# Optimization experiments

Measured on AMD Instinct MI355X. Metric: run time of the kernel, lower is better.

## Reference

```python
import jax, jax.numpy as jnp
import numpy as np

N = 100000
IN_DIM = 128
OUT_DIM = 128
E = 3200000


def setup_inputs() -> dict:
    key = jax.random.key(0)
    k1, k2, k3, k4, k5 = jax.random.split(key, 5)
    x = jax.random.normal(k1, (N, IN_DIM), dtype=jnp.float32)
    src = jax.random.randint(k2, (E,), 0, N)
    dst = jax.random.randint(k3, (E,), 0, N)
    edge_index = jnp.stack([src, dst], axis=0)  # (2, E) int
    # Linear(2*in_dim, out_dim): torch stores weight as (out, in)
    bound = 1.0 / np.sqrt(2 * IN_DIM)
    W = jax.random.uniform(k4, (OUT_DIM, 2 * IN_DIM), minval=-bound, maxval=bound, dtype=jnp.float32)
    b = jax.random.uniform(k5, (OUT_DIM,), minval=-bound, maxval=bound, dtype=jnp.float32)
    return {"x": x, "edge_index": edge_index, "W": W, "b": b}


def reference(x, edge_index, W, b):
    # x: (N, d), edge_index: (2, E)
    n = x.shape[0]
    src, dst = edge_index[0], edge_index[1]
    # scatter-add of source features into target buckets (mean aggregation)
    agg = jax.ops.segment_sum(x[src], dst, num_segments=n)          # (N, d)
    count = jax.ops.segment_sum(jnp.ones((src.shape[0],), x.dtype), dst, num_segments=n)
    count = jnp.maximum(count, 1.0)[:, None]                         # (N, 1)
    neigh_mean = agg / count
    combined = jnp.concatenate([x, neigh_mean], axis=1)              # (N, 2d)
    return combined @ W.T + b
```

## Files before the change

kernel.cpp:

```cpp
#include <hip/hip_runtime.h>

typedef unsigned int u32;
typedef unsigned short u16;
typedef unsigned char u8;
typedef _Float16 half8 __attribute__((ext_vector_type(8)));
typedef float f32x4 __attribute__((ext_vector_type(4)));
typedef float f32x2 __attribute__((ext_vector_type(2)));

#define STRIDE 16384

__global__ __launch_bounds__(256) void part_k(const int* __restrict__ src, const int* __restrict__ dst,
                                              int E, u32* __restrict__ cnt,
                                              u32* __restrict__ packed, int nbkt,
                                              const float* __restrict__ x, u16* __restrict__ xh,
                                              u32* __restrict__ xq,
                                              const float* __restrict__ W, u16* __restrict__ wh,
                                              int N, int nba, int nbx) {
  int b = blockIdx.x, tid = threadIdx.x;
  if (b < nba) {
    __shared__ u32 h[512];
    for (int t = tid; t < 512; t += 256) h[t] = 0u;
    __syncthreads();
    int base = b * 8192;
    for (int it = 0; it < 32; it++) {
      int i = base + it * 256 + tid;
      if (i < E) atomicAdd(&h[(u32)dst[i] >> 8], 1u);
    }
    __syncthreads();
    for (int t = tid; t < nbkt; t += 256) {
      u32 c = h[t];
      h[t] = c ? atomicAdd(&cnt[t], c) : 0u;
    }
    __syncthreads();
    for (int it = 0; it < 32; it++) {
      int i = base + it * 256 + tid;
      if (i < E) {
        u32 d = (u32)dst[i];
        u32 pos = atomicAdd(&h[d >> 8], 1u);
        if (pos < (u32)STRIDE)
          packed[(size_t)(d >> 8) * STRIDE + pos] = (u32)src[i] | ((d & 255u) << 24);
      }
    }
  } else if (b < nba + nbx) {
    int i = (b - nba) * 256 + tid;
    if (i < N * 32) {
      const float4 v = *(const float4*)(x + (size_t)i * 4);
      u32 p0 = __builtin_bit_cast(u32, __builtin_amdgcn_cvt_pkrtz(v.x, v.y));
      u32 p1 = __builtin_bit_cast(u32, __builtin_amdgcn_cvt_pkrtz(v.z, v.w));
      *(uint2*)(xh + (size_t)i * 4) = uint2{p0, p1};
      u32 q = 0;
      q = __builtin_amdgcn_cvt_pk_fp8_f32(v.x, v.y, q, false);
      q = __builtin_amdgcn_cvt_pk_fp8_f32(v.z, v.w, q, true);
      xq[i] = q;
    }
  } else {
    int i = (b - nba - nbx) * 256 + tid;
    if (i < 8192) {
      const float4 v = *(const float4*)(W + (size_t)i * 4);
      u32 p0 = __builtin_bit_cast(u32, __builtin_amdgcn_cvt_pkrtz(v.x, v.y));
      u32 p1 = __builtin_bit_cast(u32, __builtin_amdgcn_cvt_pkrtz(v.z, v.w));
      *(uint2*)(wh + (size_t)i * 4) = uint2{p0, p1};
    }
  }
}

__global__ __launch_bounds__(256) void bucket_k(const u32* __restrict__ packed,
                                                const u32* __restrict__ cnt, int N,
                                                u32* __restrict__ offsets, int* __restrict__ ssrc,
                                                u8* __restrict__ nodeperm) {
  __shared__ u32 c256[256];
  __shared__ u32 scn[256];
  __shared__ u32 cur[256];
  int b = blockIdx.x, t = threadIdx.x;
  size_t fb = (size_t)b * STRIDE;
  u32 cb = cnt[b]; if (cb > (u32)STRIDE) cb = (u32)STRIDE;
  c256[t] = 0u;
  __syncthreads();
  for (u32 j = t; j < cb; j += 256) atomicAdd(&c256[packed[fb + j] >> 24], 1u);
  __syncthreads();
  u32 v = c256[t];
  scn[t] = v;
  __syncthreads();
  for (int off = 1; off < 256; off <<= 1) {
    u32 x = (t >= off) ? scn[t - off] : 0u;
    __syncthreads();
    scn[t] += x;
    __syncthreads();
  }
  u32 lbase = scn[t] - v;
  int node = b * 256 + t;
  int lastT = N - 1 - b * 256; if (lastT > 255) lastT = 255;
  u32* orow = offsets + (size_t)b * 257;
  if (node < N) {
    orow[t] = (u32)(fb + lbase);
    if (t == lastT) orow[t + 1] = (u32)(fb + lbase + v);
  }
  cur[t] = lbase;
  __syncthreads();
  for (u32 j = t; j < cb; j += 256) {
    u32 w = packed[fb + j];
    u32 pos = atomicAdd(&cur[w >> 24], 1u);
    ssrc[fb + pos] = (int)(w & 0xFFFFFFu);
  }
  {
    int g = t >> 5, l = t & 31;
    u32 mykey = c256[t] * 256u + (u32)l;
    const u32* cg = &c256[g * 32];
    u32 rank = 0;
#pragma unroll 8
    for (int l2 = 0; l2 < 32; l2++) {
      u32 k2 = cg[l2] * 256u + (u32)l2;
      rank += (k2 < mykey) ? 1u : 0u;
    }
    nodeperm[(size_t)b * 256 + g * 32 + rank] = (u8)l;
  }
}

#define DECV(vv, A0, A1, A2, A3) { f32x2 p;                              \
    p = __builtin_amdgcn_cvt_pk_f32_fp8((vv).x, false); A0 += p;         \
    p = __builtin_amdgcn_cvt_pk_f32_fp8((vv).x, true);  A1 += p;         \
    p = __builtin_amdgcn_cvt_pk_f32_fp8((vv).y, false); A2 += p;         \
    p = __builtin_amdgcn_cvt_pk_f32_fp8((vv).y, true);  A3 += p; }

__global__ __launch_bounds__(256) void fuse_k(const int* __restrict__ ssrc,
                                              const u32* __restrict__ offsets,
                                              const u32* __restrict__ xq,
                                              const u16* __restrict__ xh,
                                              const u16* __restrict__ wh,
                                              const float* __restrict__ bias,
                                              const u8* __restrict__ nodeperm,
                                              float* __restrict__ out, int N) {
  __shared__ u16 mlds[32][136];
  int wv = threadIdx.x >> 6, lane = threadIdx.x & 63;
  int sub = lane >> 4, cl = lane & 15;
  int nbase = blockIdx.x * 32;

  for (int r = 0; r < 2; r++) {
    int ln = nodeperm[(size_t)nbase + r * 16 + wv * 4 + sub];
    int node = nbase + ln;
    f32x2 A0{0.f,0.f}, A1{0.f,0.f}, A2{0.f,0.f}, A3{0.f,0.f};
    u32 deg = 0;
    if (node < N) {
      size_t oi = (size_t)(node >> 8) * 257 + (node & 255);
      u32 s0 = offsets[oi], s1 = offsets[oi + 1];
      deg = s1 - s0;
      u32 j = s0;
      u32 nq = deg >> 2;
      if (nq) {
        uint4 iA = *(const uint4*)(ssrc + j);
        for (u32 q = 1; q < nq; q++) {
          uint4 iN = *(const uint4*)(ssrc + j + 4);
          uint2 v0 = *(const uint2*)(xq + ((size_t)iA.x << 5) + (cl << 1));
          uint2 v1 = *(const uint2*)(xq + ((size_t)iA.y << 5) + (cl << 1));
          uint2 v2 = *(const uint2*)(xq + ((size_t)iA.z << 5) + (cl << 1));
          uint2 v3 = *(const uint2*)(xq + ((size_t)iA.w << 5) + (cl << 1));
          DECV(v0, A0, A1, A2, A3) DECV(v1, A0, A1, A2, A3)
          DECV(v2, A0, A1, A2, A3) DECV(v3, A0, A1, A2, A3)
          iA = iN; j += 4;
        }
        {
          uint2 v0 = *(const uint2*)(xq + ((size_t)iA.x << 5) + (cl << 1));
          uint2 v1 = *(const uint2*)(xq + ((size_t)iA.y << 5) + (cl << 1));
          uint2 v2 = *(const uint2*)(xq + ((size_t)iA.z << 5) + (cl << 1));
          uint2 v3 = *(const uint2*)(xq + ((size_t)iA.w << 5) + (cl << 1));
          DECV(v0, A0, A1, A2, A3) DECV(v1, A0, A1, A2, A3)
          DECV(v2, A0, A1, A2, A3) DECV(v3, A0, A1, A2, A3)
          j += 4;
        }
      }
      for (; j < s1; j++) {
        int e = ssrc[j];
        uint2 v = *(const uint2*)(xq + ((size_t)e << 5) + (cl << 1));
        DECV(v, A0, A1, A2, A3)
      }
    }
    float inv = 1.0f / (float)(deg ? deg : 1u);
    u32 o0 = __builtin_bit_cast(u32, __builtin_amdgcn_cvt_pkrtz(A0.x * inv, A0.y * inv));
    u32 o1 = __builtin_bit_cast(u32, __builtin_amdgcn_cvt_pkrtz(A1.x * inv, A1.y * inv));
    u32 o2 = __builtin_bit_cast(u32, __builtin_amdgcn_cvt_pkrtz(A2.x * inv, A2.y * inv));
    u32 o3 = __builtin_bit_cast(u32, __builtin_amdgcn_cvt_pkrtz(A3.x * inv, A3.y * inv));
    *(uint4*)&mlds[ln][cl * 8] = uint4{o0, o1, o2, o3};
  }
  __syncthreads();

  int la = lane & 15, lb = lane >> 4;
  int strip = wv & 1, ch = wv >> 1;
  int rbase = nbase + strip * 16;
  half8 a[8];
  const u16* ab = xh + ((size_t)(rbase + la) << 7) + lb * 8;
#pragma unroll
  for (int kb = 0; kb < 4; kb++) a[kb] = *(const half8*)(ab + kb * 32);
#pragma unroll
  for (int kb = 0; kb < 4; kb++)
    a[4 + kb] = *(const half8*)(&mlds[strip * 16 + la][kb * 32 + lb * 8]);

#pragma unroll
  for (int c = 0; c < 4; c++) {
    int ct = ch * 4 + c;
    f32x4 acc = { 0.f, 0.f, 0.f, 0.f };
    const u16* bbase = wh + ((size_t)(ct * 16 + la) << 8) + lb * 8;
#pragma unroll
    for (int kb = 0; kb < 8; kb++) {
      half8 b = *(const half8*)(bbase + kb * 32);
      acc = __builtin_amdgcn_mfma_f32_16x16x32_f16(a[kb], b, acc, 0, 0, 0);
    }
    float bc = bias[ct * 16 + la];
#pragma unroll
    for (int jj = 0; jj < 4; jj++) {
      int rr = rbase + lb * 4 + jj;
      if (rr < N) out[((size_t)rr << 7) + ct * 16 + la] = acc[jj] + bc;
    }
  }
}

extern "C" void kernel_launch(void* const* d_in, const int* in_sizes, int n_in,
                              void* d_out, int out_size, void* d_ws, size_t ws_size,
                              hipStream_t stream) {
  const float* x    = (const float*)d_in[0];
  const int*   ei   = (const int*)d_in[1];
  const float* W    = (const float*)d_in[2];
  const float* bias = (const float*)d_in[3];
  const int N = in_sizes[0] / 128;
  const int E = in_sizes[1] / 2;
  const int nbkt = (N + 255) >> 8;
  const int* src = ei;
  const int* dst = ei + E;
  float* out = (float*)d_out;

  u32* packed = (u32*)d_out;

  char* ws = (char*)d_ws;
  int* ssrc = (int*)ws;
  size_t off = ((size_t)nbkt * STRIDE * 4 + 255) & ~(size_t)255;
  u32* cnt = (u32*)(ws + off);
  u32* offsets = cnt + nbkt;
  off += ((size_t)(nbkt + nbkt * 257) * 4 + 255) & ~(size_t)255;
  off = (off + 255) & ~(size_t)255;
  u16* xh = (u16*)(ws + off);
  off += (size_t)N * 128 * 2;
  off = (off + 255) & ~(size_t)255;
  u32* xq = (u32*)(ws + off);
  off += (size_t)N * 128;
  off = (off + 255) & ~(size_t)255;
  u16* wh = (u16*)(ws + off);
  off += (size_t)128 * 256 * 2;
  off = (off + 255) & ~(size_t)255;
  u8* nodeperm = (u8*)(ws + off);

  const int nbx = (N * 32 + 255) / 256;
  const int nba = (E + 8191) / 8192;
  hipMemsetAsync(cnt, 0, (size_t)nbkt * 4, stream);
  part_k<<<nba + nbx + 32, 256, 0, stream>>>(src, dst, E, cnt, packed, nbkt,
                                             x, xh, xq, W, wh, N, nba, nbx);
  bucket_k<<<nbkt, 256, 0, stream>>>(packed, cnt, N, offsets, ssrc, nodeperm);
  fuse_k<<<(N + 31) / 32, 256, 0, stream>>>(ssrc, offsets, xq, xh, wh, bias, nodeperm, out, N);
}
```

Baseline: 188.7 us.

## Split fp8 feature table into column quarters and gather per quarter

Stores the fp8-quantized feature matrix as four column-quarter planes of 32 bytes per row instead of one 128-byte row. The gather kernel now gives each 8-lane group one node and loops over the four planes, loading 4 bytes per lane instead of 8. Each pass therefore touches a smaller plane, which may raise cache hit rates for the random neighbor gathers. In exchange every node's index list is re-read four times and each load is narrower, so per-edge instruction and index overhead roughly quadruples.

```diff
diff --git a/kernel.cpp b/kernel.cpp
--- a/kernel.cpp
+++ b/kernel.cpp
@@ -51,7 +51,9 @@
       u32 q = 0;
       q = __builtin_amdgcn_cvt_pk_fp8_f32(v.x, v.y, q, false);
       q = __builtin_amdgcn_cvt_pk_fp8_f32(v.z, v.w, q, true);
-      xq[i] = q;
+      int row = i >> 5, c = i & 31;
+      int qt = c >> 3, w = c & 7;
+      xq[(size_t)qt * (N * 8) + (size_t)row * 8 + w] = q;
     }
   } else {
     int i = (b - nba - nbx) * 256 + tid;
@@ -116,11 +118,9 @@
   }
 }
 
-#define DECV(vv, A0, A1, A2, A3) { f32x2 p;                              \
-    p = __builtin_amdgcn_cvt_pk_f32_fp8((vv).x, false); A0 += p;         \
-    p = __builtin_amdgcn_cvt_pk_f32_fp8((vv).x, true);  A1 += p;         \
-    p = __builtin_amdgcn_cvt_pk_f32_fp8((vv).y, false); A2 += p;         \
-    p = __builtin_amdgcn_cvt_pk_f32_fp8((vv).y, true);  A3 += p; }
+#define DEC1(vv, P0, P1) { f32x2 p;                                      \
+    p = __builtin_amdgcn_cvt_pk_f32_fp8((vv), false); P0 += p;           \
+    p = __builtin_amdgcn_cvt_pk_f32_fp8((vv), true);  P1 += p; }
 
 __global__ __launch_bounds__(256) void fuse_k(const int* __restrict__ ssrc,
                                               const u32* __restrict__ offsets,
@@ -132,54 +132,54 @@
                                               float* __restrict__ out, int N) {
   __shared__ u16 mlds[32][136];
   int wv = threadIdx.x >> 6, lane = threadIdx.x & 63;
-  int sub = lane >> 4, cl = lane & 15;
+  int sg = lane >> 3, c8 = lane & 7;
   int nbase = blockIdx.x * 32;
 
-  for (int r = 0; r < 2; r++) {
-    int ln = nodeperm[(size_t)nbase + r * 16 + wv * 4 + sub];
-    int node = nbase + ln;
-    f32x2 A0{0.f,0.f}, A1{0.f,0.f}, A2{0.f,0.f}, A3{0.f,0.f};
-    u32 deg = 0;
+  int ln = nodeperm[(size_t)nbase + wv * 8 + sg];
+  int node = nbase + ln;
+  u32 s0 = 0, s1 = 0;
+  if (node < N) {
+    size_t oi = (size_t)(node >> 8) * 257 + (node & 255);
+    s0 = offsets[oi]; s1 = offsets[oi + 1];
+  }
+  u32 deg = s1 - s0;
+  float inv = 1.0f / (float)(deg ? deg : 1u);
+
+#pragma unroll 1
+  for (int p = 0; p < 4; p++) {
+    const u32* xqp = xq + (size_t)p * ((size_t)N * 8);
+    f32x2 P0{0.f, 0.f}, P1{0.f, 0.f};
     if (node < N) {
-      size_t oi = (size_t)(node >> 8) * 257 + (node & 255);
-      u32 s0 = offsets[oi], s1 = offsets[oi + 1];
-      deg = s1 - s0;
       u32 j = s0;
       u32 nq = deg >> 2;
       if (nq) {
         uint4 iA = *(const uint4*)(ssrc + j);
         for (u32 q = 1; q < nq; q++) {
           uint4 iN = *(const uint4*)(ssrc + j + 4);
-          uint2 v0 = *(const uint2*)(xq + ((size_t)iA.x << 5) + (cl << 1));
-          uint2 v1 = *(const uint2*)(xq + ((size_t)iA.y << 5) + (cl << 1));
-          uint2 v2 = *(const uint2*)(xq + ((size_t)iA.z << 5) + (cl << 1));
-          uint2 v3 = *(const uint2*)(xq + ((size_t)iA.w << 5) + (cl << 1));
-          DECV(v0, A0, A1, A2, A3) DECV(v1, A0, A1, A2, A3)
-          DECV(v2, A0, A1, A2, A3) DECV(v3, A0, A1, A2, A3)
+          u32 v0 = xqp[((size_t)iA.x << 3) + c8];
+          u32 v1 = xqp[((size_t)iA.y << 3) + c8];
+          u32 v2 = xqp[((size_t)iA.z << 3) + c8];
+          u32 v3 = xqp[((size_t)iA.w << 3) + c8];
+          DEC1(v0, P0, P1) DEC1(v1, P0, P1) DEC1(v2, P0, P1) DEC1(v3, P0, P1)
           iA = iN; j += 4;
         }
         {
-          uint2 v0 = *(const uint2*)(xq + ((size_t)iA.x << 5) + (cl << 1));
-          uint2 v1 = *(const uint2*)(xq + ((size_t)iA.y << 5) + (cl << 1));
-          uint2 v2 = *(const uint2*)(xq + ((size_t)iA.z << 5) + (cl << 1));
-          uint2 v3 = *(const uint2*)(xq + ((size_t)iA.w << 5) + (cl << 1));
-          DECV(v0, A0, A1, A2, A3) DECV(v1, A0, A1, A2, A3)
-          DECV(v2, A0, A1, A2, A3) DECV(v3, A0, A1, A2, A3)
+          u32 v0 = xqp[((size_t)iA.x << 3) + c8];
+          u32 v1 = xqp[((size_t)iA.y << 3) + c8];
+          u32 v2 = xqp[((size_t)iA.z << 3) + c8];
+          u32 v3 = xqp[((size_t)iA.w << 3) + c8];
+          DEC1(v0, P0, P1) DEC1(v1, P0, P1) DEC1(v2, P0, P1) DEC1(v3, P0, P1)
           j += 4;
         }
       }
       for (; j < s1; j++) {
-        int e = ssrc[j];
-        uint2 v = *(const uint2*)(xq + ((size_t)e << 5) + (cl << 1));
-        DECV(v, A0, A1, A2, A3)
+        u32 v = xqp[((size_t)(u32)ssrc[j] << 3) + c8];
+        DEC1(v, P0, P1)
       }
     }
-    float inv = 1.0f / (float)(deg ? deg : 1u);
-    u32 o0 = __builtin_bit_cast(u32, __builtin_amdgcn_cvt_pkrtz(A0.x * inv, A0.y * inv));
-    u32 o1 = __builtin_bit_cast(u32, __builtin_amdgcn_cvt_pkrtz(A1.x * inv, A1.y * inv));
-    u32 o2 = __builtin_bit_cast(u32, __builtin_amdgcn_cvt_pkrtz(A2.x * inv, A2.y * inv));
-    u32 o3 = __builtin_bit_cast(u32, __builtin_amdgcn_cvt_pkrtz(A3.x * inv, A3.y * inv));
-    *(uint4*)&mlds[ln][cl * 8] = uint4{o0, o1, o2, o3};
+    u32 o0 = __builtin_bit_cast(u32, __builtin_amdgcn_cvt_pkrtz(P0.x * inv, P0.y * inv));
+    u32 o1 = __builtin_bit_cast(u32, __builtin_amdgcn_cvt_pkrtz(P1.x * inv, P1.y * inv));
+    *(uint2*)&mlds[ln][p * 32 + c8 * 4] = uint2{o0, o1};
   }
   __syncthreads();
 
```

Measured after the change: 255.0 us. +35.1%, slower.
